# Kernel optimization log

Measured on AMD Instinct MI355X. Metric: run time of the kernel, lower is better.

## Reference

```python
import jax, jax.numpy as jnp
import numpy as np

VOCAB = 28996
B, W, D, H = 16, 64, 256, 512


def setup_inputs() -> dict:
    key = jax.random.key(0)
    ks = jax.random.split(key, 8)
    s_ih = 1.0 / np.sqrt(H)
    return {
        "x": jax.random.normal(ks[0], (B, W, D), dtype=jnp.float32),
        "last_encoder_hidden_state": jax.random.normal(ks[1], (1, H), dtype=jnp.float32),
        "w_ih": jax.random.uniform(ks[2], (3 * H, D), jnp.float32, -s_ih, s_ih),
        "w_hh": jax.random.uniform(ks[3], (3 * H, H), jnp.float32, -s_ih, s_ih),
        "b_ih": jax.random.uniform(ks[4], (3 * H,), jnp.float32, -s_ih, s_ih),
        "b_hh": jax.random.uniform(ks[5], (3 * H,), jnp.float32, -s_ih, s_ih),
        "w_pred": jax.random.uniform(ks[6], (VOCAB, H), jnp.float32, -s_ih, s_ih),
        "b_pred": jax.random.uniform(ks[7], (VOCAB,), jnp.float32, -s_ih, s_ih),
    }


def reference(x, last_encoder_hidden_state, w_ih, w_hh, b_ih, b_hh, w_pred, b_pred):
    b, w, d = x.shape
    # The torch code carries a single [1,H] hidden state sequentially over ALL
    # batch rows and words (state flows across batch boundaries). Flatten to T steps.
    xf = x.reshape(b * w, d)
    xg = xf @ w_ih.T + b_ih  # [T, 3H] input gate pre-activations, batched GEMM

    def step(h, xg_t):
        gh = h @ w_hh.T + b_hh            # [3H]
        xr, xz, xn = jnp.split(xg_t, 3)
        hr, hz, hn = jnp.split(gh, 3)
        r = jax.nn.sigmoid(xr + hr)
        z = jax.nn.sigmoid(xz + hz)
        n = jnp.tanh(xn + r * hn)
        h_new = (1.0 - z) * n + z * h
        return h_new, h_new

    h0 = last_encoder_hidden_state[0]     # [H]
    _, hs = jax.lax.scan(step, h0, xg)    # hs: [T, H]
    preds = hs @ w_pred.T + b_pred        # [T, VOCAB]
    return preds.reshape(b, w, VOCAB)
```

## Files before the change

kernel.cpp:

```cpp
#include <hip/hip_runtime.h>
#include <hip/hip_bf16.h>
#include <cstdint>

#define VOCAB 28996
#define T_STEPS 1024
#define D_IN 256
#define HDIM 512

using f32x4 = __attribute__((ext_vector_type(4))) float;
using s16x8 = __attribute__((ext_vector_type(8))) short;

static __device__ __forceinline__ unsigned short f2bf(float f){
    unsigned u = __float_as_uint(f);
    u = u + 0x7FFFu + ((u >> 16) & 1u);
    return (unsigned short)(u >> 16);
}

#define SENT_U 0x7FC00001u

__global__ void init_hs_kernel(const float* __restrict__ h0, float* __restrict__ hs,
                               unsigned* __restrict__ ctrl){
    const int col = threadIdx.x;
    const int row = blockIdx.x;
    float v = (row == 0) ? h0[col] : __uint_as_float(SENT_U);
    hs[(size_t)row * HDIM + col] = v;
    if (row == 0 && col < 8) ctrl[col] = 0u;
}

__global__ void xg_kernel(const float* __restrict__ x, const float* __restrict__ w_ih,
                          const float* __restrict__ b_ih, float* __restrict__ xg){
    __shared__ float xs[8][D_IN];
    const int tid = threadIdx.x;
    const int i   = blockIdx.x * 256 + tid;
    const int t0  = blockIdx.y * 8;
    #pragma unroll
    for (int r = 0; r < 8; ++r)
        xs[r][tid] = x[(size_t)(t0 + r) * D_IN + tid];
    __syncthreads();

    float acc[8] = {0.f,0.f,0.f,0.f,0.f,0.f,0.f,0.f};
    const float* wrow = w_ih + (size_t)i * D_IN;
    for (int d = 0; d < D_IN; d += 4){
        float4 w4 = *(const float4*)(wrow + d);
        #pragma unroll
        for (int r = 0; r < 8; ++r){
            acc[r] += w4.x * xs[r][d]   + w4.y * xs[r][d+1]
                    + w4.z * xs[r][d+2] + w4.w * xs[r][d+3];
        }
    }
    const float b = b_ih[i];
    #pragma unroll
    for (int r = 0; r < 8; ++r)
        xg[(size_t)(t0 + r) * (3*HDIM) + i] = acc[r] + b;
}

#define LDW(G, P, n) \
    float G##n##0 = (P)[64*n + 0], G##n##1 = (P)[64*n + 1], \
          G##n##2 = (P)[64*n + 2], G##n##3 = (P)[64*n + 3];
#define PINW(G, n) \
    asm volatile("" : "+v"(G##n##0), "+v"(G##n##1), "+v"(G##n##2), "+v"(G##n##3));

#define GSTEP(n, arx, azx, anx) { \
    float4 h4 = *(const float4*)&hbuf[wv][4*c + 64*n]; \
    arx += R##n##0*h4.x + R##n##1*h4.y + R##n##2*h4.z + R##n##3*h4.w; \
    azx += Z##n##0*h4.x + Z##n##1*h4.y + Z##n##2*h4.z + Z##n##3*h4.w; \
    anx += N##n##0*h4.x + N##n##1*h4.y + N##n##2*h4.z + N##n##3*h4.w; }

__launch_bounds__(512, 1)
__global__ void scan_kernel(const float* __restrict__ xg, const float* __restrict__ w_hh,
                            const float* __restrict__ b_hh, float* hs, unsigned* ctrl){
    __shared__ __align__(16) float hbuf[8][HDIM];
    __shared__ unsigned sh_rank;

    const int tid = threadIdx.x;
    if (tid == 0){
        unsigned xcc;
        asm volatile("s_getreg_b32 %0, hwreg(HW_REG_XCC_ID)" : "=s"(xcc));
        sh_rank = __hip_atomic_fetch_add(&ctrl[xcc & 7u], 1u, __ATOMIC_RELAXED,
                                         __HIP_MEMORY_SCOPE_AGENT);
    }
    __syncthreads();
    const unsigned rank = sh_rank;
    if (rank >= 16u) return;

    const int wv   = tid >> 6;
    const int lane = tid & 63;
    const int c    = tid & 15;
    const int jl   = tid >> 4;
    const int j    = (int)rank * 32 + jl;

    const float* wrp = w_hh + (size_t)j * HDIM + 4*c;
    const float* wzp = w_hh + (size_t)(HDIM   + j) * HDIM + 4*c;
    const float* wnp = w_hh + (size_t)(2*HDIM + j) * HDIM + 4*c;
    LDW(R, wrp, 0) LDW(R, wrp, 1) LDW(R, wrp, 2) LDW(R, wrp, 3)
    LDW(R, wrp, 4) LDW(R, wrp, 5) LDW(R, wrp, 6) LDW(R, wrp, 7)
    LDW(Z, wzp, 0) LDW(Z, wzp, 1) LDW(Z, wzp, 2) LDW(Z, wzp, 3)
    LDW(Z, wzp, 4) LDW(Z, wzp, 5) LDW(Z, wzp, 6) LDW(Z, wzp, 7)
    LDW(N, wnp, 0) LDW(N, wnp, 1) LDW(N, wnp, 2) LDW(N, wnp, 3)
    LDW(N, wnp, 4) LDW(N, wnp, 5) LDW(N, wnp, 6) LDW(N, wnp, 7)
    PINW(R,0) PINW(R,1) PINW(R,2) PINW(R,3) PINW(R,4) PINW(R,5) PINW(R,6) PINW(R,7)
    PINW(Z,0) PINW(Z,1) PINW(Z,2) PINW(Z,3) PINW(Z,4) PINW(Z,5) PINW(Z,6) PINW(Z,7)
    PINW(N,0) PINW(N,1) PINW(N,2) PINW(N,3) PINW(N,4) PINW(N,5) PINW(N,6) PINW(N,7)

    float bhr = b_hh[j], bhz = b_hh[HDIM + j], bhn = b_hh[2*HDIM + j];
    asm volatile("" : "+v"(bhr), "+v"(bhz), "+v"(bhn));

    float xr_c = 0.f, xz_c = 0.f, xn_c = 0.f;
    if (c == 0){ xr_c = xg[j]; xz_c = xg[HDIM + j]; xn_c = xg[2*HDIM + j]; }

    #pragma unroll 1
    for (int t = 0; t < T_STEPS; ++t){
        const float4* myp = (const float4*)(hs + (size_t)t * HDIM) + lane;
        float4 va, vb;
        int spins = 0;
        for (;;){
            asm volatile("global_load_dwordx4 %0, %2, off nt\n\t"
                         "global_load_dwordx4 %1, %2, off offset:1024 nt\n\t"
                         "s_waitcnt vmcnt(0)"
                         : "=&v"(va), "=&v"(vb) : "v"(myp) : "memory");
            int ok = (__float_as_uint(va.x) != SENT_U) & (__float_as_uint(va.y) != SENT_U)
                   & (__float_as_uint(va.z) != SENT_U) & (__float_as_uint(va.w) != SENT_U)
                   & (__float_as_uint(vb.x) != SENT_U) & (__float_as_uint(vb.y) != SENT_U)
                   & (__float_as_uint(vb.z) != SENT_U) & (__float_as_uint(vb.w) != SENT_U);
            if (__all(ok)) break;
            if (++spins > 5000) return;
        }

        float xr_n = 0.f, xz_n = 0.f, xn_n = 0.f;
        if (c == 0 && t + 1 < T_STEPS){
            const float* xgn = xg + (size_t)(t + 1) * (3*HDIM);
            xr_n = xgn[j]; xz_n = xgn[HDIM + j]; xn_n = xgn[2*HDIM + j];
        }

        *(float4*)&hbuf[wv][4 * lane]       = va;
        *(float4*)&hbuf[wv][256 + 4 * lane] = vb;
        asm volatile("s_waitcnt lgkmcnt(0)" ::: "memory");
        __builtin_amdgcn_sched_barrier(0);

        float ar0=0.f, ar1=0.f, az0=0.f, az1=0.f, an0=0.f, an1=0.f;
        GSTEP(0, ar0, az0, an0)  GSTEP(1, ar1, az1, an1)
        GSTEP(2, ar0, az0, an0)  GSTEP(3, ar1, az1, an1)
        GSTEP(4, ar0, az0, an0)  GSTEP(5, ar1, az1, an1)
        GSTEP(6, ar0, az0, an0)  GSTEP(7, ar1, az1, an1)
        float ar = ar0 + ar1, az = az0 + az1, an = an0 + an1;
        #pragma unroll
        for (int m = 1; m < 16; m <<= 1){
            ar += __shfl_xor(ar, m);
            az += __shfl_xor(az, m);
            an += __shfl_xor(an, m);
        }

        if (c == 0){
            const float r  = 1.0f / (1.0f + __expf(-(xr_c + ar + bhr)));
            const float z  = 1.0f / (1.0f + __expf(-(xz_c + az + bhz)));
            const float nn = xn_c + r * (an + bhn);
            const float e  = __expf(2.0f * nn);
            const float th = 1.0f - 2.0f / (e + 1.0f);
            const float hnew = (1.0f - z) * th + z * hbuf[wv][j];
            hs[(size_t)(t + 1) * HDIM + j] = hnew;
        }
        xr_c = xr_n; xz_c = xz_n; xn_c = xn_n;
    }
}

__launch_bounds__(256)
__global__ void pred_gemm_kernel(const float* __restrict__ hs, const float* __restrict__ w_pred,
                                 const float* __restrict__ b_pred, float* __restrict__ out){
    __shared__ unsigned short As[128 * 32];
    __shared__ unsigned short Bs[128 * 32];
    const int tid   = threadIdx.x;
    const int mtile = blockIdx.x;
    const int ntile = blockIdx.y;
    const int row  = tid >> 1, half = tid & 1;
    const int wave = tid >> 6, lane = tid & 63;
    const int wm = wave >> 1, wn = wave & 1;
    const int lr = lane & 15, kq = lane >> 4;

    f32x4 acc[4][4] = {};

    const float* Abase = hs + HDIM  + (size_t)(mtile * 128 + row) * HDIM;
    const int    nrow  = ntile * 128 + row;
    const float* Bbase = w_pred + (size_t)nrow * HDIM;

    for (int k0 = 0; k0 < HDIM; k0 += 32){
        {
            const float* srcp = Abase + k0 + half * 16;
            unsigned short* dst = &As[row * 32 + half * 16];
            #pragma unroll
            for (int q = 0; q < 4; ++q){
                float4 v = *(const float4*)(srcp + 4 * q);
                uint2 p;
                p.x = (unsigned)f2bf(v.x) | ((unsigned)f2bf(v.y) << 16);
                p.y = (unsigned)f2bf(v.z) | ((unsigned)f2bf(v.w) << 16);
                *(uint2*)(dst + 4 * q) = p;
            }
        }
        {
            unsigned short* dst = &Bs[row * 32 + half * 16];
            if (nrow < VOCAB){
                const float* srcp = Bbase + k0 + half * 16;
                #pragma unroll
                for (int q = 0; q < 4; ++q){
                    float4 v = *(const float4*)(srcp + 4 * q);
                    uint2 p;
                    p.x = (unsigned)f2bf(v.x) | ((unsigned)f2bf(v.y) << 16);
                    p.y = (unsigned)f2bf(v.z) | ((unsigned)f2bf(v.w) << 16);
                    *(uint2*)(dst + 4 * q) = p;
                }
            } else {
                uint2 zz; zz.x = 0u; zz.y = 0u;
                #pragma unroll
                for (int q = 0; q < 4; ++q) *(uint2*)(dst + 4 * q) = zz;
            }
        }
        __syncthreads();

        const unsigned short* Ab = &As[(wm * 64 + lr) * 32 + kq * 8];
        const unsigned short* Bb = &Bs[(wn * 64 + lr) * 32 + kq * 8];
        s16x8 af[4], bf[4];
        #pragma unroll
        for (int mf = 0; mf < 4; ++mf) af[mf] = *(const s16x8*)(Ab + mf * 16 * 32);
        #pragma unroll
        for (int nf = 0; nf < 4; ++nf) bf[nf] = *(const s16x8*)(Bb + nf * 16 * 32);
        #pragma unroll
        for (int mf = 0; mf < 4; ++mf){
            #pragma unroll
            for (int nf = 0; nf < 4; ++nf){
                acc[mf][nf] = __builtin_amdgcn_mfma_f32_16x16x32_bf16(af[mf], bf[nf], acc[mf][nf], 0, 0, 0);
            }
        }
        __syncthreads();
    }

    #pragma unroll
    for (int nf = 0; nf < 4; ++nf){
        const int n = ntile * 128 + wn * 64 + nf * 16 + lr;
        if (n >= VOCAB) continue;
        const float bp = b_pred[n];
        #pragma unroll
        for (int mf = 0; mf < 4; ++mf){
            const int m = mtile * 128 + wm * 64 + mf * 16 + kq * 4;
            #pragma unroll
            for (int q = 0; q < 4; ++q){
                out[(size_t)(m + q) * VOCAB + n] = acc[mf][nf][q] + bp;
            }
        }
    }
}

extern "C" void kernel_launch(void* const* d_in, const int* in_sizes, int n_in,
                              void* d_out, int out_size, void* d_ws, size_t ws_size,
                              hipStream_t stream){
    const float* x      = (const float*)d_in[0];
    const float* h0     = (const float*)d_in[1];
    const float* w_ih   = (const float*)d_in[2];
    const float* w_hh   = (const float*)d_in[3];
    const float* b_ih   = (const float*)d_in[4];
    const float* b_hh   = (const float*)d_in[5];
    const float* w_pred = (const float*)d_in[6];
    const float* b_pred = (const float*)d_in[7];
    float* out = (float*)d_out;

    float*    xg   = (float*)d_ws;
    float*    hs   = xg + (size_t)T_STEPS * (3*HDIM);
    unsigned* ctrl = (unsigned*)(hs + (size_t)(T_STEPS+1) * HDIM);

    hipLaunchKernelGGL(init_hs_kernel, dim3(T_STEPS + 1), dim3(HDIM), 0, stream, h0, hs, ctrl);
    hipLaunchKernelGGL(xg_kernel,      dim3(6, 128),      dim3(256),  0, stream, x, w_ih, b_ih, xg);
    hipLaunchKernelGGL(scan_kernel,    dim3(128),         dim3(512),  0, stream, xg, w_hh, b_hh, hs, ctrl);
    hipLaunchKernelGGL(pred_gemm_kernel, dim3(8, 227),    dim3(256),  0, stream, hs, w_pred, b_pred, out);
}
```

Before: 1.775 ms.

## Spread GRU scan over twice the blocks with single-wave polling and LDS handoff

The recurrent scan kernel now uses 32 blocks per XCC, each owning 16 hidden units, instead of 16 blocks owning 32. That halves the per-thread weight registers and dot-product work per step, at the cost of one more shuffle reduction stage. Only wave 0 now polls global memory for the previous hidden state. It copies that state into a double-buffered LDS slot and publishes the step number through a shared flag that the other waves spin on. This replaces eight waves per block all polling global memory, cutting polling traffic, but adds an intra-block spin handoff and depends on enough blocks landing on each XCC.

```diff
diff --git a/kernel.cpp b/kernel.cpp
--- a/kernel.cpp
+++ b/kernel.cpp
@@ -54,23 +54,24 @@
         xg[(size_t)(t0 + r) * (3*HDIM) + i] = acc[r] + b;
 }
 
-#define LDW(G, P, n) \
-    float G##n##0 = (P)[64*n + 0], G##n##1 = (P)[64*n + 1], \
-          G##n##2 = (P)[64*n + 2], G##n##3 = (P)[64*n + 3];
-#define PINW(G, n) \
-    asm volatile("" : "+v"(G##n##0), "+v"(G##n##1), "+v"(G##n##2), "+v"(G##n##3));
-
-#define GSTEP(n, arx, azx, anx) { \
-    float4 h4 = *(const float4*)&hbuf[wv][4*c + 64*n]; \
-    arx += R##n##0*h4.x + R##n##1*h4.y + R##n##2*h4.z + R##n##3*h4.w; \
-    azx += Z##n##0*h4.x + Z##n##1*h4.y + Z##n##2*h4.z + Z##n##3*h4.w; \
-    anx += N##n##0*h4.x + N##n##1*h4.y + N##n##2*h4.z + N##n##3*h4.w; }
+#define LDW(G, P, s) \
+    float G##s##0 = (P)[128*s + 0], G##s##1 = (P)[128*s + 1], \
+          G##s##2 = (P)[128*s + 2], G##s##3 = (P)[128*s + 3];
+#define PINW(G, s) \
+    asm volatile("" : "+v"(G##s##0), "+v"(G##s##1), "+v"(G##s##2), "+v"(G##s##3));
+
+#define GSTEP(s, arx, azx, anx) { \
+    float4 h4 = *(const float4*)&hcur[4*c + 128*s]; \
+    arx += R##s##0*h4.x + R##s##1*h4.y + R##s##2*h4.z + R##s##3*h4.w; \
+    azx += Z##s##0*h4.x + Z##s##1*h4.y + Z##s##2*h4.z + Z##s##3*h4.w; \
+    anx += N##s##0*h4.x + N##s##1*h4.y + N##s##2*h4.z + N##s##3*h4.w; }
 
 __launch_bounds__(512, 1)
 __global__ void scan_kernel(const float* __restrict__ xg, const float* __restrict__ w_hh,
                             const float* __restrict__ b_hh, float* hs, unsigned* ctrl){
-    __shared__ __align__(16) float hbuf[8][HDIM];
+    __shared__ __align__(16) float hbuf[2][HDIM];
     __shared__ unsigned sh_rank;
+    __shared__ int sh_step;
 
     const int tid = threadIdx.x;
     if (tid == 0){
@@ -78,29 +79,27 @@
         asm volatile("s_getreg_b32 %0, hwreg(HW_REG_XCC_ID)" : "=s"(xcc));
         sh_rank = __hip_atomic_fetch_add(&ctrl[xcc & 7u], 1u, __ATOMIC_RELAXED,
                                          __HIP_MEMORY_SCOPE_AGENT);
+        sh_step = -1;
     }
     __syncthreads();
     const unsigned rank = sh_rank;
-    if (rank >= 16u) return;
+    if (rank >= 32u) return;
 
     const int wv   = tid >> 6;
     const int lane = tid & 63;
-    const int c    = tid & 15;
-    const int jl   = tid >> 4;
-    const int j    = (int)rank * 32 + jl;
+    const int c    = tid & 31;
+    const int jl   = tid >> 5;
+    const int j    = (int)rank * 16 + jl;
 
     const float* wrp = w_hh + (size_t)j * HDIM + 4*c;
     const float* wzp = w_hh + (size_t)(HDIM   + j) * HDIM + 4*c;
     const float* wnp = w_hh + (size_t)(2*HDIM + j) * HDIM + 4*c;
     LDW(R, wrp, 0) LDW(R, wrp, 1) LDW(R, wrp, 2) LDW(R, wrp, 3)
-    LDW(R, wrp, 4) LDW(R, wrp, 5) LDW(R, wrp, 6) LDW(R, wrp, 7)
     LDW(Z, wzp, 0) LDW(Z, wzp, 1) LDW(Z, wzp, 2) LDW(Z, wzp, 3)
-    LDW(Z, wzp, 4) LDW(Z, wzp, 5) LDW(Z, wzp, 6) LDW(Z, wzp, 7)
     LDW(N, wnp, 0) LDW(N, wnp, 1) LDW(N, wnp, 2) LDW(N, wnp, 3)
-    LDW(N, wnp, 4) LDW(N, wnp, 5) LDW(N, wnp, 6) LDW(N, wnp, 7)
-    PINW(R,0) PINW(R,1) PINW(R,2) PINW(R,3) PINW(R,4) PINW(R,5) PINW(R,6) PINW(R,7)
-    PINW(Z,0) PINW(Z,1) PINW(Z,2) PINW(Z,3) PINW(Z,4) PINW(Z,5) PINW(Z,6) PINW(Z,7)
-    PINW(N,0) PINW(N,1) PINW(N,2) PINW(N,3) PINW(N,4) PINW(N,5) PINW(N,6) PINW(N,7)
+    PINW(R,0) PINW(R,1) PINW(R,2) PINW(R,3)
+    PINW(Z,0) PINW(Z,1) PINW(Z,2) PINW(Z,3)
+    PINW(N,0) PINW(N,1) PINW(N,2) PINW(N,3)
 
     float bhr = b_hh[j], bhz = b_hh[HDIM + j], bhn = b_hh[2*HDIM + j];
     asm volatile("" : "+v"(bhr), "+v"(bhz), "+v"(bhn));
@@ -110,21 +109,46 @@
 
     #pragma unroll 1
     for (int t = 0; t < T_STEPS; ++t){
-        const float4* myp = (const float4*)(hs + (size_t)t * HDIM) + lane;
-        float4 va, vb;
-        int spins = 0;
-        for (;;){
-            asm volatile("global_load_dwordx4 %0, %2, off nt\n\t"
-                         "global_load_dwordx4 %1, %2, off offset:1024 nt\n\t"
-                         "s_waitcnt vmcnt(0)"
-                         : "=&v"(va), "=&v"(vb) : "v"(myp) : "memory");
-            int ok = (__float_as_uint(va.x) != SENT_U) & (__float_as_uint(va.y) != SENT_U)
-                   & (__float_as_uint(va.z) != SENT_U) & (__float_as_uint(va.w) != SENT_U)
-                   & (__float_as_uint(vb.x) != SENT_U) & (__float_as_uint(vb.y) != SENT_U)
-                   & (__float_as_uint(vb.z) != SENT_U) & (__float_as_uint(vb.w) != SENT_U);
-            if (__all(ok)) break;
-            if (++spins > 5000) return;
-        }
+        float* hcur = hbuf[t & 1];
+
+        if (wv == 0){
+            const float4* myp = (const float4*)(hs + (size_t)t * HDIM) + lane;
+            float4 va, vb;
+            int spins = 0, dead = 0;
+            for (;;){
+                asm volatile("global_load_dwordx4 %0, %2, off nt\n\t"
+                             "global_load_dwordx4 %1, %2, off offset:1024 nt\n\t"
+                             "s_waitcnt vmcnt(0)"
+                             : "=&v"(va), "=&v"(vb) : "v"(myp) : "memory");
+                int ok = (__float_as_uint(va.x) != SENT_U) & (__float_as_uint(va.y) != SENT_U)
+                       & (__float_as_uint(va.z) != SENT_U) & (__float_as_uint(va.w) != SENT_U)
+                       & (__float_as_uint(vb.x) != SENT_U) & (__float_as_uint(vb.y) != SENT_U)
+                       & (__float_as_uint(vb.z) != SENT_U) & (__float_as_uint(vb.w) != SENT_U);
+                if (__all(ok)) break;
+                if (++spins > 2000){ dead = 1; break; }
+            }
+            if (dead){
+                if (lane == 0)
+                    __hip_atomic_store(&sh_step, 0x7FFFFFFF, __ATOMIC_RELAXED,
+                                       __HIP_MEMORY_SCOPE_WORKGROUP);
+                return;
+            }
+            *(float4*)&hcur[4 * lane]       = va;
+            *(float4*)&hcur[256 + 4 * lane] = vb;
+            asm volatile("s_waitcnt lgkmcnt(0)" ::: "memory");
+            if (lane == 0)
+                __hip_atomic_store(&sh_step, t, __ATOMIC_RELAXED,
+                                   __HIP_MEMORY_SCOPE_WORKGROUP);
+        } else {
+            int v;
+            do {
+                v = __hip_atomic_load(&sh_step, __ATOMIC_RELAXED,
+                                      __HIP_MEMORY_SCOPE_WORKGROUP);
+            } while (v < t);
+            if (v == 0x7FFFFFFF) return;
+        }
+        asm volatile("" ::: "memory");
+        __builtin_amdgcn_sched_barrier(0);
 
         float xr_n = 0.f, xz_n = 0.f, xn_n = 0.f;
         if (c == 0 && t + 1 < T_STEPS){
@@ -132,19 +156,12 @@
             xr_n = xgn[j]; xz_n = xgn[HDIM + j]; xn_n = xgn[2*HDIM + j];
         }
 
-        *(float4*)&hbuf[wv][4 * lane]       = va;
-        *(float4*)&hbuf[wv][256 + 4 * lane] = vb;
-        asm volatile("s_waitcnt lgkmcnt(0)" ::: "memory");
-        __builtin_amdgcn_sched_barrier(0);
-
         float ar0=0.f, ar1=0.f, az0=0.f, az1=0.f, an0=0.f, an1=0.f;
         GSTEP(0, ar0, az0, an0)  GSTEP(1, ar1, az1, an1)
         GSTEP(2, ar0, az0, an0)  GSTEP(3, ar1, az1, an1)
-        GSTEP(4, ar0, az0, an0)  GSTEP(5, ar1, az1, an1)
-        GSTEP(6, ar0, az0, an0)  GSTEP(7, ar1, az1, an1)
         float ar = ar0 + ar1, az = az0 + az1, an = an0 + an1;
         #pragma unroll
-        for (int m = 1; m < 16; m <<= 1){
+        for (int m = 1; m < 32; m <<= 1){
             ar += __shfl_xor(ar, m);
             az += __shfl_xor(az, m);
             an += __shfl_xor(an, m);
@@ -156,7 +173,7 @@
             const float nn = xn_c + r * (an + bhn);
             const float e  = __expf(2.0f * nn);
             const float th = 1.0f - 2.0f / (e + 1.0f);
-            const float hnew = (1.0f - z) * th + z * hbuf[wv][j];
+            const float hnew = (1.0f - z) * th + z * hcur[j];
             hs[(size_t)(t + 1) * HDIM + j] = hnew;
         }
         xr_c = xr_n; xz_c = xz_n; xn_c = xn_n;
@@ -267,6 +284,6 @@
 
     hipLaunchKernelGGL(init_hs_kernel, dim3(T_STEPS + 1), dim3(HDIM), 0, stream, h0, hs, ctrl);
     hipLaunchKernelGGL(xg_kernel,      dim3(6, 128),      dim3(256),  0, stream, x, w_ih, b_ih, xg);
-    hipLaunchKernelGGL(scan_kernel,    dim3(128),         dim3(512),  0, stream, xg, w_hh, b_hh, hs, ctrl);
+    hipLaunchKernelGGL(scan_kernel,    dim3(256),         dim3(512),  0, stream, xg, w_hh, b_hh, hs, ctrl);
     hipLaunchKernelGGL(pred_gemm_kernel, dim3(8, 227),    dim3(256),  0, stream, hs, w_pred, b_pred, out);
 }
```

After: 1.835 ms. 3.4% more time.
